# Optimization experiments

Hardware: AMD Instinct MI355X
Metric: run time of the kernel (lower is better)

## Reference

```python
import jax, jax.numpy as jnp
import numpy as np

B, CDD, HIS, S, D, NH, FF, V, K = 8, 5, 50, 64, 768, 12, 3072, 30522, 8


def _ln(x):
    mu = x.mean(-1, keepdims=True)
    var = ((x - mu) ** 2).mean(-1, keepdims=True)
    return (x - mu) / jnp.sqrt(var + 1e-12)


def _transformer(x, mask, Wq, Wk, Wv, Wo, W1, W2):
    # x: [..., S, D]; mask: [..., S] (float, >0 means valid)
    lead = x.shape[:-2]
    s, d = x.shape[-2], x.shape[-1]
    dh = d // NH
    x2 = x.reshape(-1, s, d)
    m = mask.reshape(-1, s)
    split = lambda t: t.reshape(-1, s, NH, dh).transpose(0, 2, 1, 3)
    q, k, v = split(x2 @ Wq), split(x2 @ Wk), split(x2 @ Wv)
    logits = jnp.einsum('nhqd,nhkd->nhqk', q, k) / jnp.sqrt(jnp.float32(dh))
    logits = logits + jnp.where(m > 0, 0.0, -1e9)[:, None, None, :]
    a = jax.nn.softmax(logits, axis=-1)
    o = jnp.einsum('nhqk,nhkd->nhqd', a, v).transpose(0, 2, 1, 3).reshape(-1, s, d) @ Wo
    h = _ln(x2 + o)
    h = _ln(h + jax.nn.gelu(h @ W1) @ W2)
    h = h.reshape(*lead, s, d)
    return h, h[..., 0, :]


def _build_prefix(subword_index, mask):
    # subword_index: [B, n, S, 2] int; mask: [B, n, 1] float
    b, n = subword_index.shape[0], subword_index.shape[1]
    flat = subword_index[..., 0] * S + subword_index[..., 1]  # [B, n, S]
    dest = jnp.zeros((b * n, S * S), jnp.float32)
    dest = dest.at[jnp.arange(b * n)[:, None], flat.reshape(b * n, S)].set(1.0)
    dest = dest * mask.reshape(b * n, 1)
    prefix = dest.reshape(b, n, S, S)
    # granularity == 'avg' -> L1 normalize rows
    prefix = prefix / jnp.maximum(prefix.sum(-1, keepdims=True), 1e-12)
    return prefix


def setup_inputs() -> dict:
    key = jax.random.key(0)
    ks = jax.random.split(key, 24)
    w = lambda k, shp: jax.random.normal(k, shp, jnp.float32) * 0.02
    inp = {
        'cdd_subword_index': jax.random.randint(ks[0], (B, CDD, S, 2), 0, S, jnp.int32),
        'his_subword_index': jax.random.randint(ks[1], (B, HIS, S, 2), 0, S, jnp.int32),
        'cdd_encoded_index': jax.random.randint(ks[2], (B, CDD, S), 0, V, jnp.int32),
        'his_encoded_index': jax.random.randint(ks[3], (B, HIS, S), 0, V, jnp.int32),
        'cdd_mask': jnp.ones((B, CDD, 1), jnp.float32),
        'his_mask': jnp.ones((B, HIS, 1), jnp.float32),
        'cdd_attn_mask': jnp.ones((B, CDD, S), jnp.float32),
        'his_attn_mask': jnp.ones((B, HIS, S), jnp.float32),
        'emb': w(ks[4], (V, D)),
        'bert_Wq': w(ks[5], (D, D)), 'bert_Wk': w(ks[6], (D, D)),
        'bert_Wv': w(ks[7], (D, D)), 'bert_Wo': w(ks[8], (D, D)),
        'bert_W1': w(ks[9], (D, FF)), 'bert_W2': w(ks[10], (FF, D)),
        'encN_Wq': w(ks[11], (D, D)), 'encN_Wk': w(ks[12], (D, D)),
        'encN_Wv': w(ks[13], (D, D)), 'encN_Wo': w(ks[14], (D, D)),
        'encN_W1': w(ks[15], (D, FF)), 'encN_W2': w(ks[16], (FF, D)),
        'qU': w(ks[17], (D,)),
        'proj_W': w(ks[18], (D, D)), 'proj_b': jnp.zeros((D,), jnp.float32),
    }
    return inp


def reference(cdd_subword_index, his_subword_index, cdd_encoded_index, his_encoded_index,
              cdd_mask, his_mask, cdd_attn_mask, his_attn_mask, emb,
              bert_Wq, bert_Wk, bert_Wv, bert_Wo, bert_W1, bert_W2,
              encN_Wq, encN_Wk, encN_Wv, encN_Wo, encN_W1, encN_W2,
              qU, proj_W, proj_b):
    rt_d = jnp.sqrt(jnp.float32(D))
    # scatter-built one-hot subword->token prefix matrices
    cdd_prefix = _build_prefix(cdd_subword_index, cdd_mask)   # [B,C,S,S]
    his_prefix = _build_prefix(his_subword_index, his_mask)   # [B,H,S,S]
    # pooled attention masks: prefix @ mask
    cdd_attn = jnp.einsum('bcst,bct->bcs', cdd_prefix, cdd_attn_mask)
    his_attn = jnp.einsum('bnst,bnt->bns', his_prefix, his_attn_mask)
    # embedding lookup + subword->token pooling
    cdd_emb = jnp.einsum('bcst,bctd->bcsd', cdd_prefix, emb[cdd_encoded_index])
    his_emb = jnp.einsum('bnst,bntd->bnsd', his_prefix, emb[his_encoded_index])
    # candidate news: BERT encode, take CLS, project
    _, cdd_cls = _transformer(cdd_emb, cdd_attn, bert_Wq, bert_Wk, bert_Wv, bert_Wo, bert_W1, bert_W2)
    cdd_repr = jnp.tanh(cdd_cls @ proj_W + proj_b)            # [B,C,D]
    # history news encoder
    his_hidden, his_cls = _transformer(his_emb, his_attn, encN_Wq, encN_Wk, encN_Wv, encN_Wo, encN_W1, encN_W2)
    # user encoder: attention pooling over history news reprs
    wgt = jax.nn.softmax(jnp.einsum('bnd,d->bn', his_cls, qU) / rt_d, axis=-1)
    user0 = jnp.einsum('bn,bnd->bd', wgt, his_cls)            # [B,D]
    # matching reducer: top-k personalized terms per history news
    scores = jnp.einsum('bnsd,bd->bns', his_hidden, user0) / rt_d
    scores = jnp.where(his_attn > 0, scores, -1e9)
    _, kid = jax.lax.top_k(scores, K)                         # [B,H,K]
    ps_terms = jnp.take_along_axis(his_hidden, kid[..., None], axis=2).reshape(B, HIS * K, D)
    ps_mask = jnp.take_along_axis(his_attn, kid, axis=2).reshape(B, HIS * K)
    # user BERT over selected terms
    _, user_cls = _transformer(ps_terms, ps_mask, bert_Wq, bert_Wk, bert_Wv, bert_Wo, bert_W1, bert_W2)
    user_repr = jnp.tanh(user_cls @ proj_W + proj_b)          # [B,D]
    score = jnp.einsum('bcd,bd->bc', cdd_repr, user_repr) / rt_d
    prob = jax.nn.log_softmax(score, axis=1)
    return prob, kid
```

## Files before the change

kernel.cpp:

```cpp
#include <hip/hip_runtime.h>
#include <math.h>

#define DIM 768
#define NHEAD 12
#define DHEAD 64
#define FFDIM 3072

typedef _Float16 v8h __attribute__((ext_vector_type(8)));
typedef float v4f __attribute__((ext_vector_type(4)));

__device__ __forceinline__ float gelu_f(float x) {
    float x3 = x * x * x;
    return 0.5f * x * (1.0f + tanhf(0.7978845608028654f * (x + 0.044715f * x3)));
}

__device__ __forceinline__ void gl_lds16(const _Float16* g, _Float16* l) {
    __builtin_amdgcn_global_load_lds(
        (const __attribute__((address_space(1))) unsigned int*)(g),
        (__attribute__((address_space(3))) unsigned int*)(l),
        16, 0, 0);
}

struct GemmP {
    const _Float16* A1; const _Float16* A2;
    const _Float16* eB1[3]; const _Float16* eB2[3]; const _Float16* bB1[3];
    float* C[3];
    _Float16* G1; _Float16* G2;
    int bnd;
};

__global__ __launch_bounds__(256) void gemm_mfma(GemmP p, int M, int N, int K,
                                                 int epi, float cdiv, float gscale, int nbg)
{
    __shared__ _Float16 sm[2][3][128 * 32];
    const int tid = threadIdx.x;
    const int w = tid >> 6, lane = tid & 63;
    const int lm = lane & 15, kg = lane >> 4;

    const int nb = (int)gridDim.x, mb = (int)gridDim.y;
    const int nwg = nb * mb * (int)gridDim.z;
    int lid = (int)blockIdx.x + nb * ((int)blockIdx.y + mb * (int)blockIdx.z);
    int qd = nwg >> 3, rm = nwg & 7;
    int xcd = lid & 7, pos = lid >> 3;
    int wid = (xcd < rm ? xcd * (qd + 1) : rm * (qd + 1) + (xcd - rm) * qd) + pos;
    int gsz = (nbg > 0 && (nb % nbg) == 0) ? nbg : 1;
    int ngrp = nb / gsz;
    int bxi = wid % gsz; int tt = wid / gsz;
    int by = tt % mb; tt /= mb;
    int bxg = tt % ngrp;
    int z = tt / ngrp;
    const int row0 = by << 7, col0 = (bxg * gsz + bxi) << 7;

    const int wm = (w >> 1) << 6, wn = (w & 1) << 6;
    const int rl = (w << 4) + (lane >> 2);
    const int cofs = (((lane & 3) ^ ((lane >> 3) & 3)) << 3);
    const int ks = ((kg ^ ((lm >> 1) & 3)) << 3);
    int nt; const _Float16 *B1p, *B2p;
    if (row0 < p.bnd) { nt = 3; B1p = p.eB1[z]; B2p = p.eB2[z]; }
    else             { nt = 1; B1p = p.bB1[z]; B2p = p.bB1[z]; }
    const _Float16* A1 = p.A1 + (size_t)row0 * K;
    const _Float16* A2 = p.A2 + (size_t)row0 * K;
    const _Float16* B1 = B1p + (size_t)col0 * K;
    const _Float16* B2 = B2p + (size_t)col0 * K;
    const int ldsLo = w * 512, ldsHi = (w + 4) * 512;
    const size_t gbase = (size_t)rl * K + cofs;

    v4f acc[4][4];
#pragma unroll
    for (int i = 0; i < 4; i++)
#pragma unroll
        for (int j = 0; j < 4; j++) acc[i][j] = (v4f){0.f, 0.f, 0.f, 0.f};

    auto stage = [&](int d, int k0) {
        size_t glo = gbase + k0;
        size_t ghi = glo + (size_t)64 * K;
        gl_lds16(A1 + glo, sm[d][0] + ldsLo); gl_lds16(A1 + ghi, sm[d][0] + ldsHi);
        gl_lds16(B1 + glo, sm[d][2] + ldsLo); gl_lds16(B1 + ghi, sm[d][2] + ldsHi);
        if (nt == 3) {
            gl_lds16(A2 + glo, sm[d][1] + ldsLo); gl_lds16(A2 + ghi, sm[d][1] + ldsHi);
        }
    };

    const int nk = K >> 5;
    stage(0, 0);
    __syncthreads();
    for (int i = 0; i < nk; i++) {
        int cur = i & 1;
        int k0 = i << 5;
        v8h b2f[4];
        if (nt == 3) {
#pragma unroll
            for (int j = 0; j < 4; j++)
                b2f[j] = *(const v8h*)(B2 + (size_t)(wn + (j << 4) + lm) * K + k0 + (kg << 3));
        }
        if (i + 1 < nk) stage(cur ^ 1, (i + 1) << 5);
        const _Float16* sA1 = sm[cur][0]; const _Float16* sA2 = sm[cur][1];
        const _Float16* sB1 = sm[cur][2];
        v8h a1[4], b1f[4];
#pragma unroll
        for (int i2 = 0; i2 < 4; i2++) {
            a1[i2]  = *(const v8h*)(sA1 + (wm + (i2 << 4) + lm) * 32 + ks);
            b1f[i2] = *(const v8h*)(sB1 + (wn + (i2 << 4) + lm) * 32 + ks);
        }
#pragma unroll
        for (int i2 = 0; i2 < 4; i2++)
#pragma unroll
            for (int j = 0; j < 4; j++)
                acc[i2][j] = __builtin_amdgcn_mfma_f32_16x16x32_f16(a1[i2], b1f[j], acc[i2][j], 0, 0, 0);
        if (nt == 3) {
#pragma unroll
            for (int i2 = 0; i2 < 4; i2++)
#pragma unroll
                for (int j = 0; j < 4; j++)
                    acc[i2][j] = __builtin_amdgcn_mfma_f32_16x16x32_f16(a1[i2], b2f[j], acc[i2][j], 0, 0, 0);
            v8h a2[4];
#pragma unroll
            for (int i2 = 0; i2 < 4; i2++)
                a2[i2] = *(const v8h*)(sA2 + (wm + (i2 << 4) + lm) * 32 + ks);
#pragma unroll
            for (int i2 = 0; i2 < 4; i2++)
#pragma unroll
                for (int j = 0; j < 4; j++)
                    acc[i2][j] = __builtin_amdgcn_mfma_f32_16x16x32_f16(a2[i2], b1f[j], acc[i2][j], 0, 0, 0);
        }
        __syncthreads();
    }
    float* C = p.C[z];
#pragma unroll
    for (int i = 0; i < 4; i++) {
        int rb = row0 + wm + (i << 4) + (kg << 2);
#pragma unroll
        for (int j = 0; j < 4; j++) {
            int cc = col0 + wn + (j << 4) + lm;
#pragma unroll
            for (int r = 0; r < 4; r++) {
                float c = acc[i][j][r] * cdiv;
                size_t idx = (size_t)(rb + r) * N + cc;
                if (epi == 0) {
                    C[idx] = c;
                } else {
                    float gv = gelu_f(c) * gscale;
                    _Float16 g1 = (_Float16)gv;
                    p.G1[idx] = g1;
                    p.G2[idx] = (_Float16)(gv - (float)g1);
                }
            }
        }
    }
}

struct WJobs {
    const float* src[12];
    _Float16* d1[12]; _Float16* d2[12];
    int K[12]; int N[12]; int start[12];
};
__global__ __launch_bounds__(256) void wsplit_tr(WJobs jb)
{
    __shared__ float sh[32 * 33];
    int bid = blockIdx.x;
    int ji = 0;
#pragma unroll
    for (int i = 1; i < 12; i++) if (bid >= jb.start[i]) ji = i;
    const float* src = jb.src[ji];
    _Float16* d1 = jb.d1[ji]; _Float16* d2 = jb.d2[ji];
    int K = jb.K[ji], N = jb.N[ji];
    int t = bid - jb.start[ji];
    int tilesN = N >> 5;
    int tk = t / tilesN, tn = t - tk * tilesN;
    int k0 = tk << 5, n0 = tn << 5;
    int c = threadIdx.x & 31, rr = threadIdx.x >> 5;
#pragma unroll
    for (int pph = 0; pph < 4; pph++) {
        int r = rr + (pph << 3);
        sh[c * 33 + r] = src[(size_t)(k0 + r) * N + n0 + c];
    }
    __syncthreads();
#pragma unroll
    for (int pph = 0; pph < 4; pph++) {
        int rn = rr + (pph << 3);
        float v = sh[rn * 33 + c] * 64.f;
        _Float16 b1 = (_Float16)v;
        size_t idx = (size_t)(n0 + rn) * K + k0 + c;
        d1[idx] = b1;
        if (d2) d2[idx] = (_Float16)(v - (float)b1);
    }
}

__global__ __launch_bounds__(256) void build_prefix2(const int* __restrict__ hisSub,
    const float* __restrict__ hisMask, const float* __restrict__ hisAmask,
    const int* __restrict__ cddSub, const float* __restrict__ cddMask,
    const float* __restrict__ cddAmask,
    float* __restrict__ P, float* __restrict__ hisA, float* __restrict__ cddA)
{
    __shared__ float pref[64 * 64];
    int g = blockIdx.x;
    const int* sub; const float* mask; const float* amask; float* aout; int li;
    if (g < 400) { sub = hisSub; mask = hisMask; amask = hisAmask; aout = hisA; li = g; }
    else         { sub = cddSub; mask = cddMask; amask = cddAmask; aout = cddA; li = g - 400; }
    int tid = threadIdx.x;
    for (int t = tid; t < 4096; t += 256) pref[t] = 0.f;
    __syncthreads();
    if (tid < 64) {
        int r = sub[((size_t)li * 64 + tid) * 2 + 0];
        int c = sub[((size_t)li * 64 + tid) * 2 + 1];
        pref[(r << 6) + c] = 1.0f;
    }
    __syncthreads();
    float m = mask[li];
    int lane = tid & 63, w = tid >> 6;
    for (int s = (w << 4); s < (w << 4) + 16; s++) {
        float v = pref[(s << 6) + lane] * m;
        float rs = v;
#pragma unroll
        for (int o = 32; o; o >>= 1) rs += __shfl_down(rs, o);
        rs = __shfl(rs, 0);
        float nv = v / fmaxf(rs, 1e-12f);
        P[(((size_t)g << 6) + s) * 64 + lane] = nv;
        float av = nv * amask[((size_t)li << 6) + lane];
#pragma unroll
        for (int o = 32; o; o >>= 1) av += __shfl_down(av, o);
        if (lane == 0) aout[((size_t)li << 6) + s] = av;
    }
}

__global__ __launch_bounds__(256) void emb_pool2(const float* __restrict__ P,
    const int* __restrict__ encHis, const int* __restrict__ encCdd,
    const float* __restrict__ emb, float* __restrict__ X,
    _Float16* __restrict__ s1, _Float16* __restrict__ s2, int gOffHis, int gMid)
{
    int gl = blockIdx.x >> 2, q = blockIdx.x & 3;
    int g; const int* enc;
    if (gl < gMid) { g = gOffHis + gl; enc = encHis + (size_t)g * 64; }
    else { int gc = gl - gMid; g = 400 + gc; enc = encCdd + (size_t)gc * 64; }
    int tid = threadIdx.x;
    __shared__ float pw[16][64];
    __shared__ int tk[64];
    if (tid < 64) tk[tid] = enc[tid];
    for (int u = tid; u < 1024; u += 256) {
        int si = u >> 6, t = u & 63;
        pw[si][t] = P[((size_t)g * 64 + q * 16 + si) * 64 + t];
    }
    __syncthreads();
    float acc[16][3];
#pragma unroll
    for (int si = 0; si < 16; si++) { acc[si][0] = 0.f; acc[si][1] = 0.f; acc[si][2] = 0.f; }
    for (int t = 0; t < 64; t++) {
        const float* er = emb + (size_t)tk[t] * DIM;
        float e0 = er[tid], e1 = er[tid + 256], e2 = er[tid + 512];
#pragma unroll
        for (int si = 0; si < 16; si++) {
            float w = pw[si][t];
            acc[si][0] = fmaf(w, e0, acc[si][0]);
            acc[si][1] = fmaf(w, e1, acc[si][1]);
            acc[si][2] = fmaf(w, e2, acc[si][2]);
        }
    }
#pragma unroll
    for (int si = 0; si < 16; si++) {
        size_t base = ((size_t)gl * 64 + q * 16 + si) * DIM;
#pragma unroll
        for (int cci = 0; cci < 3; cci++) {
            int cc = tid + (cci << 8);
            float v = acc[si][cci];
            X[base + cc] = v;
            float xs = v * 64.f;
            _Float16 a = (_Float16)xs;
            s1[base + cc] = a;
            s2[base + cc] = (_Float16)(xs - (float)a);
        }
    }
}

__global__ __launch_bounds__(256) void attn_fused64(const float* __restrict__ Q,
    const float* __restrict__ Km, const float* __restrict__ V,
    const float* __restrict__ maskHis, const float* __restrict__ maskCdd, int gMid,
    _Float16* __restrict__ o1, _Float16* __restrict__ o2)
{
    __shared__ float Ks[64 * 65];
    __shared__ float Vs[64 * 65];
    __shared__ float Qs[64 * 65];
    int h = blockIdx.x % NHEAD;
    int g = blockIdx.x / NHEAD;
    const float* mrow = (g < gMid) ? maskHis + (size_t)g * 64
                                   : maskCdd + (size_t)(g - gMid) * 64;
    int tid = threadIdx.x, lane = tid & 63, w = tid >> 6;
    {
        int r = tid >> 2, c0 = (tid & 3) << 4;
        const float* qp = Q  + ((size_t)g * 64 + r) * DIM + h * DHEAD + c0;
        const float* kp = Km + ((size_t)g * 64 + r) * DIM + h * DHEAD + c0;
        const float* vp = V  + ((size_t)g * 64 + r) * DIM + h * DHEAD + c0;
#pragma unroll
        for (int u = 0; u < 16; u += 4) {
            float4 qv = *(const float4*)(qp + u);
            float4 kv = *(const float4*)(kp + u);
            float4 vv = *(const float4*)(vp + u);
            int o = r * 65 + c0 + u;
            Qs[o+0]=qv.x; Qs[o+1]=qv.y; Qs[o+2]=qv.z; Qs[o+3]=qv.w;
            Ks[o+0]=kv.x; Ks[o+1]=kv.y; Ks[o+2]=kv.z; Ks[o+3]=kv.w;
            Vs[o+0]=vv.x; Vs[o+1]=vv.y; Vs[o+2]=vv.z; Vs[o+3]=vv.w;
        }
    }
    __syncthreads();
    float mk = mrow[lane] > 0.f ? 0.f : -1e9f;
    for (int il = 0; il < 16; il++) {
        int i = (w << 4) + il;
        float d = 0.f;
        for (int t = 0; t < 64; t++) d = fmaf(Qs[i * 65 + t], Ks[lane * 65 + t], d);
        float l = d * 0.125f + mk;
        float mx = l;
#pragma unroll
        for (int o = 32; o; o >>= 1) mx = fmaxf(mx, __shfl_xor(mx, o));
        float e = expf(l - mx);
        float s = e;
#pragma unroll
        for (int o = 32; o; o >>= 1) s += __shfl_xor(s, o);
        float p = e / s;
        float acc = 0.f;
        for (int j = 0; j < 64; j++) {
            float pj = __shfl(p, j);
            acc = fmaf(pj, Vs[j * 65 + lane], acc);
        }
        size_t ob = ((size_t)g * 64 + i) * DIM + h * DHEAD + lane;
        float os = acc * 64.f;
        _Float16 h1 = (_Float16)os;
        o1[ob] = h1;
        o2[ob] = (_Float16)(os - (float)h1);
    }
}

#define SSTR 449
__global__ __launch_bounds__(256) void attn_flash400(const float* __restrict__ Q,
    const float* __restrict__ Km, const float* __restrict__ V,
    const float* __restrict__ mask, _Float16* __restrict__ o1, _Float16* __restrict__ o2)
{
    __shared__ _Float16 Kt[64 * 64];
    __shared__ float Sc[16 * SSTR];
    int qt = blockIdx.x % 25;
    int h  = (blockIdx.x / 25) % NHEAD;
    int g  = blockIdx.x / (25 * NHEAD);
    int tid = threadIdx.x, w = tid >> 6, lane = tid & 63, lm = lane & 15, kg = lane >> 4;

    v8h aq0, aq1;
    {
        const float* qp = Q + ((size_t)(g * 400 + qt * 16 + lm)) * DIM + h * DHEAD;
#pragma unroll
        for (int u = 0; u < 8; u++) {
            aq0[u] = (_Float16)qp[kg * 8 + u];
            aq1[u] = (_Float16)qp[32 + kg * 8 + u];
        }
    }
    for (int jt = 0; jt < 7; jt++) {
        int j0 = jt * 64;
        __syncthreads();
        {
            int jr = tid >> 2, c0 = (tid & 3) << 4;
            int j = j0 + jr;
            _Float16* kd = Kt + jr * 64 + c0;
            if (j < 400) {
                const float* kp = Km + ((size_t)(g * 400 + j)) * DIM + h * DHEAD + c0;
#pragma unroll
                for (int u = 0; u < 16; u++) kd[u] = (_Float16)kp[u];
            } else {
#pragma unroll
                for (int u = 0; u < 16; u++) kd[u] = (_Float16)0.f;
            }
        }
        __syncthreads();
        v8h b0, b1;
#pragma unroll
        for (int u = 0; u < 8; u++) {
            b0[u] = Kt[(w * 16 + lm) * 64 + kg * 8 + u];
            b1[u] = Kt[(w * 16 + lm) * 64 + 32 + kg * 8 + u];
        }
        v4f c = {0.f, 0.f, 0.f, 0.f};
        c = __builtin_amdgcn_mfma_f32_16x16x32_f16(aq0, b0, c, 0, 0, 0);
        c = __builtin_amdgcn_mfma_f32_16x16x32_f16(aq1, b1, c, 0, 0, 0);
        int jj = j0 + w * 16 + lm;
        float mv = (jj < 400) ? (mask[g * 400 + jj] > 0.f ? 0.f : -1e9f) : -1e9f;
#pragma unroll
        for (int r = 0; r < 4; r++)
            Sc[(kg * 4 + r) * SSTR + jj] = c[r] * 0.125f + mv;
    }
    __syncthreads();
    for (int rr = 0; rr < 4; rr++) {
        int r = w * 4 + rr;
        float mx = -INFINITY;
#pragma unroll
        for (int c7 = 0; c7 < 7; c7++) mx = fmaxf(mx, Sc[r * SSTR + c7 * 64 + lane]);
#pragma unroll
        for (int o = 32; o; o >>= 1) mx = fmaxf(mx, __shfl_xor(mx, o));
        float s = 0.f;
        float ev[7];
#pragma unroll
        for (int c7 = 0; c7 < 7; c7++) { ev[c7] = expf(Sc[r * SSTR + c7 * 64 + lane] - mx); s += ev[c7]; }
#pragma unroll
        for (int o = 32; o; o >>= 1) s += __shfl_xor(s, o);
        float inv = 1.f / s;
#pragma unroll
        for (int c7 = 0; c7 < 7; c7++) Sc[r * SSTR + c7 * 64 + lane] = ev[c7] * inv;
    }
    __syncthreads();
    v4f o = {0.f, 0.f, 0.f, 0.f};
    for (int kc = 0; kc < 14; kc++) {
        v8h a, b;
#pragma unroll
        for (int u = 0; u < 8; u++) a[u] = (_Float16)Sc[lm * SSTR + kc * 32 + kg * 8 + u];
#pragma unroll
        for (int u = 0; u < 8; u++) {
            int j = kc * 32 + kg * 8 + u;
            b[u] = (j < 400) ? (_Float16)V[((size_t)(g * 400 + j)) * DIM + h * DHEAD + w * 16 + lm]
                             : (_Float16)0.f;
        }
        o = __builtin_amdgcn_mfma_f32_16x16x32_f16(a, b, o, 0, 0, 0);
    }
#pragma unroll
    for (int r = 0; r < 4; r++) {
        int qr = qt * 16 + kg * 4 + r;
        size_t ob = ((size_t)(g * 400 + qr)) * DIM + h * DHEAD + w * 16 + lm;
        float os = o[r] * 64.f;
        _Float16 h1 = (_Float16)os;
        o1[ob] = h1; o2[ob] = (_Float16)(os - (float)h1);
    }
}

__global__ __launch_bounds__(256) void add_ln2(const float* __restrict__ X,
    const float* __restrict__ Y, float* __restrict__ outA, float* __restrict__ outB,
    int bndRow, _Float16* __restrict__ S1, _Float16* __restrict__ S2, float ss,
    float* __restrict__ cls, int clsOffA, int clsOffB, int S)
{
    int r = blockIdx.x, tid = threadIdx.x;
    size_t base = (size_t)r * DIM;
    float v0 = X[base + tid] + Y[base + tid];
    float v1 = X[base + tid + 256] + Y[base + tid + 256];
    float v2 = X[base + tid + 512] + Y[base + tid + 512];
    __shared__ float red[256];
    red[tid] = v0 + v1 + v2; __syncthreads();
    for (int o = 128; o; o >>= 1) { if (tid < o) red[tid] += red[tid + o]; __syncthreads(); }
    float mu = red[0] * (1.f / 768.f);
    __syncthreads();
    float d0 = v0 - mu, d1 = v1 - mu, d2 = v2 - mu;
    red[tid] = d0 * d0 + d1 * d1 + d2 * d2; __syncthreads();
    for (int o = 128; o; o >>= 1) { if (tid < o) red[tid] += red[tid + o]; __syncthreads(); }
    float rstd = rsqrtf(red[0] * (1.f / 768.f) + 1e-12f);
    float o0 = d0 * rstd, o1 = d1 * rstd, o2 = d2 * rstd;
    float* Out = (r < bndRow) ? outA + base : outB + (size_t)(r - bndRow) * DIM;
    Out[tid] = o0; Out[tid + 256] = o1; Out[tid + 512] = o2;
    if (S1) {
        float x0 = o0 * ss, x1 = o1 * ss, x2 = o2 * ss;
        _Float16 a0 = (_Float16)x0, a1 = (_Float16)x1, a2 = (_Float16)x2;
        S1[base + tid] = a0;        S2[base + tid] = (_Float16)(x0 - (float)a0);
        S1[base + tid + 256] = a1;  S2[base + tid + 256] = (_Float16)(x1 - (float)a1);
        S1[base + tid + 512] = a2;  S2[base + tid + 512] = (_Float16)(x2 - (float)a2);
    }
    if (cls && (r % S) == 0) {
        int g = (r < bndRow) ? clsOffA + r / S : clsOffB + (r - bndRow) / S;
        float* cd = cls + (size_t)g * DIM;
        cd[tid] = o0; cd[tid + 256] = o1; cd[tid + 512] = o2;
    }
}

__global__ __launch_bounds__(256) void gemm_kernel(const float* __restrict__ A,
    const float* __restrict__ B, float* __restrict__ C,
    int M, int N, int Kd, int epi, const float* __restrict__ bias)
{
    __shared__ float As[16][64];
    __shared__ float Bs[16][64];
    int tid = threadIdx.x;
    int tx = tid & 15, ty = tid >> 4;
    int row0 = blockIdx.y << 6, col0 = blockIdx.x << 6;
    int ar = tid >> 2, ak = (tid & 3) << 2;
    int bc = tid & 63, bk0 = tid >> 6;
    const float* Ap = A + (size_t)(row0 + ar) * Kd + ak;
    const float* Bp = B + (size_t)bk0 * N + col0 + bc;
    bool aval = (row0 + ar) < M;
    float acc[4][4];
#pragma unroll
    for (int i = 0; i < 4; i++)
#pragma unroll
        for (int j = 0; j < 4; j++) acc[i][j] = 0.f;
    for (int k0 = 0; k0 < Kd; k0 += 16) {
        float4 a4 = make_float4(0.f, 0.f, 0.f, 0.f);
        if (aval) a4 = *(const float4*)(Ap + k0);
        As[ak + 0][ar] = a4.x; As[ak + 1][ar] = a4.y;
        As[ak + 2][ar] = a4.z; As[ak + 3][ar] = a4.w;
#pragma unroll
        for (int i = 0; i < 4; i++)
            Bs[bk0 + 4 * i][bc] = Bp[(size_t)(k0 + 4 * i) * N];
        __syncthreads();
#pragma unroll
        for (int kk = 0; kk < 16; kk++) {
            float4 av = *(const float4*)&As[kk][ty << 2];
            float4 bv = *(const float4*)&Bs[kk][tx << 2];
            float aa[4] = {av.x, av.y, av.z, av.w};
            float bb[4] = {bv.x, bv.y, bv.z, bv.w};
#pragma unroll
            for (int i = 0; i < 4; i++)
#pragma unroll
                for (int j = 0; j < 4; j++)
                    acc[i][j] = fmaf(aa[i], bb[j], acc[i][j]);
        }
        __syncthreads();
    }
#pragma unroll
    for (int i = 0; i < 4; i++) {
        int r = row0 + (ty << 2) + i;
        if (r >= M) continue;
        float v[4];
#pragma unroll
        for (int j = 0; j < 4; j++) {
            float x = acc[i][j];
            if (epi == 1) x = gelu_f(x);
            else if (epi == 2) x = tanhf(x + bias[col0 + (tx << 2) + j]);
            v[j] = x;
        }
        *(float4*)(C + (size_t)r * N + col0 + (tx << 2)) = make_float4(v[0], v[1], v[2], v[3]);
    }
}

__global__ __launch_bounds__(256) void user_pool_kernel(const float* __restrict__ cls,
    const float* __restrict__ qU, float* __restrict__ user0)
{
    int b = blockIdx.x, tid = threadIdx.x;
    __shared__ float red[256];
    __shared__ float wv[64];
    const float scale = 0.03608439182435161f;
    for (int n = 0; n < 50; n++) {
        const float* cr = cls + ((size_t)(b * 50 + n)) * DIM;
        float d = 0.f;
        for (int t = tid; t < DIM; t += 256) d = fmaf(cr[t], qU[t], d);
        red[tid] = d; __syncthreads();
        for (int o = 128; o; o >>= 1) { if (tid < o) red[tid] += red[tid + o]; __syncthreads(); }
        if (tid == 0) wv[n] = red[0] * scale;
        __syncthreads();
    }
    if (tid == 0) {
        float mx = -INFINITY;
        for (int n = 0; n < 50; n++) mx = fmaxf(mx, wv[n]);
        float s = 0.f;
        for (int n = 0; n < 50; n++) { float e = expf(wv[n] - mx); wv[n] = e; s += e; }
        float inv = 1.f / s;
        for (int n = 0; n < 50; n++) wv[n] *= inv;
    }
    __syncthreads();
    for (int d = tid; d < DIM; d += 256) {
        float a = 0.f;
        for (int n = 0; n < 50; n++) a = fmaf(wv[n], cls[((size_t)(b * 50 + n)) * DIM + d], a);
        user0[(size_t)b * DIM + d] = a;
    }
}

__global__ __launch_bounds__(256) void topk_kernel(const float* __restrict__ hid,
    const float* __restrict__ user0, const float* __restrict__ attn,
    float* __restrict__ kid_f, int* __restrict__ kid_i, float* __restrict__ ps_mask)
{
    int bn = blockIdx.x;
    int b = bn / 50;
    int tid = threadIdx.x, lane = tid & 63, w = tid >> 6;
    __shared__ float sc[64];
    const float* u = user0 + (size_t)b * DIM;
    const float scale = 0.03608439182435161f;
    for (int s = w; s < 64; s += 4) {
        const float* hr = hid + ((size_t)bn * 64 + s) * DIM;
        float d = 0.f;
        for (int t = lane; t < DIM; t += 64) d = fmaf(hr[t], u[t], d);
#pragma unroll
        for (int o = 32; o; o >>= 1) d += __shfl_down(d, o);
        if (lane == 0) {
            float a = attn[(size_t)bn * 64 + s];
            sc[s] = (a > 0.f) ? d * scale : -1e9f;
        }
    }
    __syncthreads();
    if (tid == 0) {
        unsigned long long used = 0ull;
        for (int k = 0; k < 8; k++) {
            float best = -INFINITY; int bi = 0;
            for (int s = 0; s < 64; s++) {
                if ((used >> s) & 1ull) continue;
                if (sc[s] > best) { best = sc[s]; bi = s; }
            }
            used |= (1ull << bi);
            kid_i[bn * 8 + k] = bi;
            kid_f[bn * 8 + k] = (float)bi;
            ps_mask[bn * 8 + k] = attn[(size_t)bn * 64 + bi];
        }
    }
}

__global__ void gather2(const float* __restrict__ hid, const int* __restrict__ kid_i,
    float* __restrict__ X, _Float16* __restrict__ s1, _Float16* __restrict__ s2)
{
    int r = blockIdx.x, tid = threadIdx.x;
    int s = kid_i[r];
    int bn = r >> 3;
    const float* src = hid + ((size_t)bn * 64 + s) * DIM;
    size_t base = (size_t)r * DIM;
#pragma unroll
    for (int cci = 0; cci < 3; cci++) {
        int cc = tid + (cci << 8);
        float v = src[cc];
        X[base + cc] = v;
        float xs = v * 64.f;
        _Float16 a = (_Float16)xs;
        s1[base + cc] = a;
        s2[base + cc] = (_Float16)(xs - (float)a);
    }
}

__global__ __launch_bounds__(256) void final_kernel(const float* __restrict__ cdd_repr,
    const float* __restrict__ user_repr, float* __restrict__ out)
{
    int b = blockIdx.x, tid = threadIdx.x;
    __shared__ float red[256];
    __shared__ float sc[5];
    const float scale = 0.03608439182435161f;
    for (int c = 0; c < 5; c++) {
        const float* cr = cdd_repr + ((size_t)(b * 5 + c)) * DIM;
        const float* ur = user_repr + (size_t)b * DIM;
        float d = 0.f;
        for (int t = tid; t < DIM; t += 256) d = fmaf(cr[t], ur[t], d);
        red[tid] = d; __syncthreads();
        for (int o = 128; o; o >>= 1) { if (tid < o) red[tid] += red[tid + o]; __syncthreads(); }
        if (tid == 0) sc[c] = red[0] * scale;
        __syncthreads();
    }
    if (tid == 0) {
        float mx = -INFINITY;
        for (int c = 0; c < 5; c++) mx = fmaxf(mx, sc[c]);
        float s = 0.f;
        for (int c = 0; c < 5; c++) s += expf(sc[c] - mx);
        float lse = logf(s) + mx;
        for (int c = 0; c < 5; c++) out[b * 5 + c] = sc[c] - lse;
    }
}

extern "C" void kernel_launch(void* const* d_in, const int* in_sizes, int n_in,
                              void* d_out, int out_size, void* d_ws, size_t ws_size,
                              hipStream_t stream)
{
    (void)in_sizes; (void)n_in; (void)out_size;
    const int*   cdd_sub   = (const int*)d_in[0];
    const int*   his_sub   = (const int*)d_in[1];
    const int*   cdd_enc   = (const int*)d_in[2];
    const int*   his_enc   = (const int*)d_in[3];
    const float* cdd_mask  = (const float*)d_in[4];
    const float* his_mask  = (const float*)d_in[5];
    const float* cdd_amask = (const float*)d_in[6];
    const float* his_amask = (const float*)d_in[7];
    const float* emb = (const float*)d_in[8];
    const float* bWsrc[6] = {(const float*)d_in[9],  (const float*)d_in[10], (const float*)d_in[11],
                             (const float*)d_in[12], (const float*)d_in[13], (const float*)d_in[14]};
    const float* eWsrc[6] = {(const float*)d_in[15], (const float*)d_in[16], (const float*)d_in[17],
                             (const float*)d_in[18], (const float*)d_in[19], (const float*)d_in[20]};
    const float* qU = (const float*)d_in[21];
    const float* pW = (const float*)d_in[22];
    const float* pb = (const float*)d_in[23];
    float* out = (float*)d_out;

    auto al256 = [](size_t b) { return (b + 255) & ~(size_t)255; };
    auto needBytes = [&](size_t RCx) -> size_t {
        size_t t = 0;
        t += 4 * al256(RCx * 768 * 4);
        t += 2 * al256(RCx * 768 * 2);
        t += al256(RCx * 3072 * 2);
        t += al256((size_t)440 * 4096 * 4);
        t += al256((size_t)400 * 64 * 768 * 4);
        t += al256((size_t)448 * 768 * 4);
        t += 8 * al256(131072);
        t += 3 * (4 * al256((size_t)589824 * 2) + 2 * al256((size_t)2359296 * 2));
        return t;
    };
    const int NSopts[9] = {400, 200, 134, 100, 66, 50, 34, 24, 10};
    int NS = 10;
    for (int i = 0; i < 9; i++) {
        size_t RCt = (size_t)NSopts[i] * 64 + 2560;
        if (needBytes(RCt) <= ws_size) { NS = NSopts[i]; break; }
    }
    const size_t RC = (size_t)NS * 64 + 2560;

    char* wsb = (char*)d_ws;
    size_t off = 0;
    auto allocB = [&](size_t bytes) { char* p = wsb + off; off += al256(bytes); return p; };
    float* R_X = (float*)allocB(RC * 768 * 4);
    float* R_Q = (float*)allocB(RC * 768 * 4);
    float* R_K = (float*)allocB(RC * 768 * 4);
    float* R_V = (float*)allocB(RC * 768 * 4);
    _Float16* s1h = (_Float16*)allocB(RC * 768 * 2);
    _Float16* s2h = (_Float16*)allocB(RC * 768 * 2);
    _Float16* g2h = (_Float16*)allocB(RC * 3072 * 2);
    float* Pa   = (float*)allocB((size_t)440 * 4096 * 4);
    float* hisH = (float*)allocB((size_t)400 * 64 * 768 * 4);
    float* cls  = (float*)allocB((size_t)448 * 768 * 4);
    float* userC = (float*)allocB(131072);
    float* hisA  = (float*)allocB(131072);
    float* cddA  = (float*)allocB(131072);
    float* cddR  = (float*)allocB(131072);
    float* userR = (float*)allocB(131072);
    float* user0 = (float*)allocB(131072);
    float* psM   = (float*)allocB(131072);
    int*   kidI  = (int*)allocB(131072);
    size_t wsz[6] = {589824, 589824, 589824, 589824, 2359296, 2359296};
    _Float16 *eB1s[6], *eB2s[6], *bB1s[6];
    for (int i = 0; i < 6; i++) eB1s[i] = (_Float16*)allocB(wsz[i] * 2);
    for (int i = 0; i < 6; i++) eB2s[i] = (_Float16*)allocB(wsz[i] * 2);
    for (int i = 0; i < 6; i++) bB1s[i] = (_Float16*)allocB(wsz[i] * 2);
    _Float16* g1h = (_Float16*)R_K;
    float* cddTrash = (float*)g2h;

    int wk[6] = {768, 768, 768, 768, 768, 3072};
    int wn[6] = {768, 768, 768, 768, 3072, 768};
    {
        WJobs jb{};
        int st = 0;
        for (int i = 0; i < 6; i++) {
            jb.src[i] = eWsrc[i]; jb.d1[i] = eB1s[i]; jb.d2[i] = eB2s[i];
            jb.K[i] = wk[i]; jb.N[i] = wn[i]; jb.start[i] = st;
            st += (wk[i] >> 5) * (wn[i] >> 5);
        }
        for (int i = 0; i < 6; i++) {
            jb.src[6 + i] = bWsrc[i]; jb.d1[6 + i] = bB1s[i]; jb.d2[6 + i] = nullptr;
            jb.K[6 + i] = wk[i]; jb.N[6 + i] = wn[i]; jb.start[6 + i] = st;
            st += (wk[i] >> 5) * (wn[i] >> 5);
        }
        wsplit_tr<<<st, 256, 0, stream>>>(jb);
    }

    build_prefix2<<<440, 256, 0, stream>>>(his_sub, his_mask, his_amask,
                                           cdd_sub, cdd_mask, cdd_amask, Pa, hisA, cddA);

    auto mkP = [&](int sl, int bnd) {
        GemmP g{};
        g.A1 = s1h; g.A2 = s2h;
        for (int z = 0; z < 3; z++) {
            g.eB1[z] = eB1s[sl]; g.eB2[z] = eB2s[sl]; g.bB1[z] = bB1s[sl];
        }
        g.bnd = bnd;
        return g;
    };

    auto tf = [&](int M, int bnd, int nseqTot, int gMid, const float* mHis,
                  float* outA, float* outB, float* clsArena, int clsOffA, int clsOffB,
                  int S, bool userAttn) {
        int MB = M >> 7;
        GemmP gq = mkP(0, bnd);
        for (int z = 0; z < 3; z++) { gq.eB1[z] = eB1s[z]; gq.eB2[z] = eB2s[z]; gq.bB1[z] = bB1s[z]; }
        gq.C[0] = R_Q; gq.C[1] = R_K; gq.C[2] = R_V;
        gemm_mfma<<<dim3(6, MB, 3), 256, 0, stream>>>(gq, M, 768, 768, 0, 1.f / 4096.f, 0.f, 6);
        if (!userAttn) {
            attn_fused64<<<nseqTot * NHEAD, 256, 0, stream>>>(R_Q, R_K, R_V, mHis, cddA, gMid, s1h, s2h);
        } else {
            attn_flash400<<<8 * NHEAD * 25, 256, 0, stream>>>(R_Q, R_K, R_V, mHis, s1h, s2h);
        }
        GemmP go = mkP(3, bnd);
        go.C[0] = R_Q;
        gemm_mfma<<<dim3(6, MB, 1), 256, 0, stream>>>(go, M, 768, 768, 0, 1.f / 4096.f, 0.f, 6);
        add_ln2<<<M, 256, 0, stream>>>(R_X, R_Q, R_X, R_X, M, s1h, s2h, 1.f, nullptr, 0, 0, 64);
        GemmP g1 = mkP(4, bnd);
        g1.G1 = g1h; g1.G2 = g2h;
        gemm_mfma<<<dim3(24, MB, 1), 256, 0, stream>>>(g1, M, 3072, 768, 1, 1.f / 64.f, 16.f, 6);
        GemmP g2 = mkP(5, bnd);
        g2.A1 = g1h; g2.A2 = g2h; g2.C[0] = R_Q;
        gemm_mfma<<<dim3(6, MB, 1), 256, 0, stream>>>(g2, M, 768, 3072, 0, 1.f / 1024.f, 0.f, 2);
        add_ln2<<<M, 256, 0, stream>>>(R_X, R_Q, outA, outB, bnd, nullptr, nullptr, 0.f,
                                       clsArena, clsOffA, clsOffB, S);
    };

    int done = 0;
    bool first = true;
    while (done < 400) {
        int ns = NS < (400 - done) ? NS : (400 - done);
        int hisRows = ns * 64;
        int M = hisRows + (first ? 2560 : 0);
        int nseqTot = ns + (first ? 40 : 0);
        emb_pool2<<<nseqTot * 4, 256, 0, stream>>>(Pa, his_enc, cdd_enc, emb, R_X, s1h, s2h, done, ns);
        tf(M, hisRows, nseqTot, ns, hisA + (size_t)done * 64,
           hisH + (size_t)done * 64 * DIM, cddTrash, cls, done, 400, 64, false);
        done += ns;
        first = false;
    }

    gemm_kernel<<<dim3(12, 1), 256, 0, stream>>>(cls + (size_t)400 * 768, pW, cddR, 40, 768, 768, 2, pb);

    user_pool_kernel<<<8, 256, 0, stream>>>(cls, qU, user0);
    topk_kernel<<<400, 256, 0, stream>>>(hisH, user0, hisA, out + 40, kidI, psM);
    gather2<<<3200, 256, 0, stream>>>(hisH, kidI, R_X, s1h, s2h);

    tf(3200, 0, 8, 0, psM, hisH, hisH, userC, 0, 0, 400, true);
    gemm_kernel<<<dim3(12, 1), 256, 0, stream>>>(userC, pW, userR, 8, 768, 768, 2, pb);

    final_kernel<<<8, 256, 0, stream>>>(cddR, userR, out);
}
```

Measured before the change: 3.362 ms.

## Triple-buffer A tiles in LDS and register-prefetch B in GEMM k-loop

Rewrites the MFMA GEMM main loop as a templated kloop specialised on the number of fp16 split terms. A tiles go through a three-stage LDS ring filled by global_load_lds. B fragments are now read straight from global memory into double-buffered registers instead of being staged in LDS. __syncthreads is replaced by explicit s_waitcnt vmcnt plus s_barrier, so loads for step i+2 can stay in flight during the compute of step i. This aims to hide global load latency and cut LDS traffic and barrier stalls. The cost is more per-wave global traffic for B, higher register pressure, and a dependence on exact vmcnt counting and on an even nk.

```diff
diff --git a/kernel.cpp b/kernel.cpp
--- a/kernel.cpp
+++ b/kernel.cpp
@@ -29,10 +29,100 @@
     int bnd;
 };
 
+template<int NT>
+__device__ __forceinline__ void kloop(
+    const _Float16* __restrict__ A1, const _Float16* __restrict__ A2,
+    const _Float16* __restrict__ B1, const _Float16* __restrict__ B2,
+    _Float16* sm, int nk, int K,
+    size_t gbase, int ldsLo, int ldsHi,
+    int wm, int wn, int lm, int kg, int ks,
+    v4f (&acc)[4][4])
+{
+    auto stageA = [&](int b, int kt) {
+        _Float16* d = sm + b * 8192;
+        size_t glo = gbase + (size_t)(kt << 5);
+        size_t ghi = glo + (size_t)64 * K;
+        gl_lds16(A1 + glo, d + ldsLo); gl_lds16(A1 + ghi, d + ldsHi);
+        if (NT == 3) {
+            gl_lds16(A2 + glo, d + 4096 + ldsLo); gl_lds16(A2 + ghi, d + 4096 + ldsHi);
+        }
+    };
+    const _Float16* pB1[4]; const _Float16* pB2[4];
+#pragma unroll
+    for (int j = 0; j < 4; j++) {
+        pB1[j] = B1 + (size_t)(wn + (j << 4) + lm) * K + (kg << 3);
+        pB2[j] = (NT == 3) ? B2 + (size_t)(wn + (j << 4) + lm) * K + (kg << 3) : pB1[j];
+    }
+    v8h b1A[4], b2A[4], b1B[4], b2B[4];
+    auto loadB = [&](v8h (&b1)[4], v8h (&b2)[4], int kt) {
+        int ko = kt << 5;
+#pragma unroll
+        for (int j = 0; j < 4; j++) b1[j] = *(const v8h*)(pB1[j] + ko);
+        if (NT == 3) {
+#pragma unroll
+            for (int j = 0; j < 4; j++) b2[j] = *(const v8h*)(pB2[j] + ko);
+        }
+    };
+
+    stageA(0, 0);
+    __builtin_amdgcn_sched_barrier(0);
+    loadB(b1A, b2A, 0);
+    __builtin_amdgcn_sched_barrier(0);
+    stageA(1, 1);
+    if (NT == 3) asm volatile("s_waitcnt vmcnt(4)\n\ts_barrier" ::: "memory");
+    else         asm volatile("s_waitcnt vmcnt(2)\n\ts_barrier" ::: "memory");
+
+    int cb = 0;
+    auto step = [&](int i, v8h (&bc1)[4], v8h (&bc2)[4], v8h (&bn1)[4], v8h (&bn2)[4]) {
+        if (i + 1 < nk) loadB(bn1, bn2, i + 1);
+        __builtin_amdgcn_sched_barrier(0);
+        int tb = cb + 2; if (tb >= 3) tb -= 3;
+        if (i + 2 < nk) stageA(tb, i + 2);
+        const _Float16* sA1 = sm + cb * 8192;
+        v8h a1[4];
+#pragma unroll
+        for (int i2 = 0; i2 < 4; i2++)
+            a1[i2] = *(const v8h*)(sA1 + (wm + (i2 << 4) + lm) * 32 + ks);
+#pragma unroll
+        for (int i2 = 0; i2 < 4; i2++)
+#pragma unroll
+            for (int j = 0; j < 4; j++)
+                acc[i2][j] = __builtin_amdgcn_mfma_f32_16x16x32_f16(a1[i2], bc1[j], acc[i2][j], 0, 0, 0);
+        if (NT == 3) {
+#pragma unroll
+            for (int i2 = 0; i2 < 4; i2++)
+#pragma unroll
+                for (int j = 0; j < 4; j++)
+                    acc[i2][j] = __builtin_amdgcn_mfma_f32_16x16x32_f16(a1[i2], bc2[j], acc[i2][j], 0, 0, 0);
+            const _Float16* sA2 = sA1 + 4096;
+            v8h a2[4];
+#pragma unroll
+            for (int i2 = 0; i2 < 4; i2++)
+                a2[i2] = *(const v8h*)(sA2 + (wm + (i2 << 4) + lm) * 32 + ks);
+#pragma unroll
+            for (int i2 = 0; i2 < 4; i2++)
+#pragma unroll
+                for (int j = 0; j < 4; j++)
+                    acc[i2][j] = __builtin_amdgcn_mfma_f32_16x16x32_f16(a2[i2], bc1[j], acc[i2][j], 0, 0, 0);
+        }
+        if (i + 2 < nk) {
+            if (NT == 3) asm volatile("s_waitcnt vmcnt(4)\n\ts_barrier" ::: "memory");
+            else         asm volatile("s_waitcnt vmcnt(2)\n\ts_barrier" ::: "memory");
+        } else if (i + 1 < nk) {
+            asm volatile("s_waitcnt vmcnt(0)\n\ts_barrier" ::: "memory");
+        }
+        cb = cb + 1; if (cb >= 3) cb = 0;
+    };
+    for (int i = 0; i < nk; i += 2) {
+        step(i,     b1A, b2A, b1B, b2B);
+        step(i + 1, b1B, b2B, b1A, b2A);
+    }
+}
+
 __global__ __launch_bounds__(256) void gemm_mfma(GemmP p, int M, int N, int K,
                                                  int epi, float cdiv, float gscale, int nbg)
 {
-    __shared__ _Float16 sm[2][3][128 * 32];
+    __shared__ _Float16 sm[3 * 8192];
     const int tid = threadIdx.x;
     const int w = tid >> 6, lane = tid & 63;
     const int lm = lane & 15, kg = lane >> 4;
@@ -71,60 +161,10 @@
 #pragma unroll
         for (int j = 0; j < 4; j++) acc[i][j] = (v4f){0.f, 0.f, 0.f, 0.f};
 
-    auto stage = [&](int d, int k0) {
-        size_t glo = gbase + k0;
-        size_t ghi = glo + (size_t)64 * K;
-        gl_lds16(A1 + glo, sm[d][0] + ldsLo); gl_lds16(A1 + ghi, sm[d][0] + ldsHi);
-        gl_lds16(B1 + glo, sm[d][2] + ldsLo); gl_lds16(B1 + ghi, sm[d][2] + ldsHi);
-        if (nt == 3) {
-            gl_lds16(A2 + glo, sm[d][1] + ldsLo); gl_lds16(A2 + ghi, sm[d][1] + ldsHi);
-        }
-    };
-
     const int nk = K >> 5;
-    stage(0, 0);
-    __syncthreads();
-    for (int i = 0; i < nk; i++) {
-        int cur = i & 1;
-        int k0 = i << 5;
-        v8h b2f[4];
-        if (nt == 3) {
-#pragma unroll
-            for (int j = 0; j < 4; j++)
-                b2f[j] = *(const v8h*)(B2 + (size_t)(wn + (j << 4) + lm) * K + k0 + (kg << 3));
-        }
-        if (i + 1 < nk) stage(cur ^ 1, (i + 1) << 5);
-        const _Float16* sA1 = sm[cur][0]; const _Float16* sA2 = sm[cur][1];
-        const _Float16* sB1 = sm[cur][2];
-        v8h a1[4], b1f[4];
-#pragma unroll
-        for (int i2 = 0; i2 < 4; i2++) {
-            a1[i2]  = *(const v8h*)(sA1 + (wm + (i2 << 4) + lm) * 32 + ks);
-            b1f[i2] = *(const v8h*)(sB1 + (wn + (i2 << 4) + lm) * 32 + ks);
-        }
-#pragma unroll
-        for (int i2 = 0; i2 < 4; i2++)
-#pragma unroll
-            for (int j = 0; j < 4; j++)
-                acc[i2][j] = __builtin_amdgcn_mfma_f32_16x16x32_f16(a1[i2], b1f[j], acc[i2][j], 0, 0, 0);
-        if (nt == 3) {
-#pragma unroll
-            for (int i2 = 0; i2 < 4; i2++)
-#pragma unroll
-                for (int j = 0; j < 4; j++)
-                    acc[i2][j] = __builtin_amdgcn_mfma_f32_16x16x32_f16(a1[i2], b2f[j], acc[i2][j], 0, 0, 0);
-            v8h a2[4];
-#pragma unroll
-            for (int i2 = 0; i2 < 4; i2++)
-                a2[i2] = *(const v8h*)(sA2 + (wm + (i2 << 4) + lm) * 32 + ks);
-#pragma unroll
-            for (int i2 = 0; i2 < 4; i2++)
-#pragma unroll
-                for (int j = 0; j < 4; j++)
-                    acc[i2][j] = __builtin_amdgcn_mfma_f32_16x16x32_f16(a2[i2], b1f[j], acc[i2][j], 0, 0, 0);
-        }
-        __syncthreads();
-    }
+    if (nt == 3) kloop<3>(A1, A2, B1, B2, sm, nk, K, gbase, ldsLo, ldsHi, wm, wn, lm, kg, ks, acc);
+    else         kloop<1>(A1, A2, B1, B2, sm, nk, K, gbase, ldsLo, ldsHi, wm, wn, lm, kg, ks, acc);
+
     float* C = p.C[z];
 #pragma unroll
     for (int i = 0; i < 4; i++) {
```

Measured after the change: 4.614 ms. +37.2%, slower.
